# Kernel optimization log

Measured on AMD Instinct MI355X. Metric: run time of the kernel, lower is better.

Reference implementation:

```python
import jax, jax.numpy as jnp
import numpy as np
from jax import lax

B, CI, CO, H, W = 8, 128, 256, 56, 56
P, K = 9, 3  # num_paths, kernel_size


def setup_inputs() -> dict:
    key = jax.random.key(0)
    ks = jax.random.split(key, 7)
    s_conv = 1.0 / np.sqrt(CI * K * K)
    s_o1 = 1.0 / np.sqrt(CI)
    s_o2 = 1.0 / np.sqrt(CO // 2)
    return {
        "x": jax.random.normal(ks[0], (B, CI, H, W), dtype=jnp.float32),
        # num_paths independent 3x3 convs, stacked on leading axis
        "kw": jax.random.uniform(ks[1], (P, CO, CI, K, K), jnp.float32, -s_conv, s_conv),
        "kb": jax.random.uniform(ks[2], (P, CO), jnp.float32, -s_conv, s_conv),
        # observer: 1x1 conv CI -> CO//2, tanh, 1x1 conv CO//2 -> P
        "ow1": jax.random.uniform(ks[3], (CO // 2, CI), jnp.float32, -s_o1, s_o1),
        "ob1": jax.random.uniform(ks[4], (CO // 2,), jnp.float32, -s_o1, s_o1),
        "ow2": jax.random.uniform(ks[5], (P, CO // 2), jnp.float32, -s_o2, s_o2),
        "ob2": jax.random.uniform(ks[6], (P,), jnp.float32, -s_o2, s_o2),
    }


def reference(x, kw, kb, ow1, ob1, ow2, ob2):
    p, co, ci, k, _ = kw.shape
    b, _, h, w = x.shape
    # All num_paths convs as a single grouped-output conv: (P*CO, CI, K, K)
    wflat = kw.reshape(p * co, ci, k, k)
    paths = lax.conv_general_dilated(
        x, wflat, window_strides=(1, 1), padding=((1, 1), (1, 1)),
        dimension_numbers=("NCHW", "OIHW", "NCHW"))
    paths = paths + kb.reshape(p * co)[None, :, None, None]
    paths = paths.reshape(b, p, co, h, w)  # [B,P,CO,H,W]

    # observer: two 1x1 convs (pure channel mixes) with tanh in between
    hmid = jnp.tanh(jnp.einsum("bchw,dc->bdhw", x, ow1) + ob1[None, :, None, None])
    scores = jnp.einsum("bdhw,pd->bphw", hmid, ow2) + ob2[None, :, None, None]

    # eval-mode collapse: argmax over paths, pixel-wise hard selection.
    # (one-hot multiply + sum over paths == gather of the winning path)
    idx = jnp.argmax(scores, axis=1)  # [B,H,W]
    out = jnp.take_along_axis(paths, idx[:, None, None, :, :], axis=1)[:, 0]  # [B,CO,H,W]
    return jax.nn.relu(out)  # norm_type='none' -> identity norm
```

## Files before the change

### kernel.cpp

```cpp
#include <hip/hip_runtime.h>
#include <hip/hip_bf16.h>


typedef unsigned int u32;

#define NPIX    25088
#define XPAD_DW (8*58*58*64)
#define OFF_LIST 4096
#define OFF_XPAD 907264
#define OFF_W2   (907264 + 6889472)

__device__ __forceinline__ unsigned short f2bf(float f) {
  u32 u = __builtin_bit_cast(u32, f);
  u32 r = (u + 0x7FFFu + ((u >> 16) & 1u)) >> 16;
  return (unsigned short)r;
}

#define GLDS16(g, l)                                                        \
  __builtin_amdgcn_global_load_lds(                                         \
      (const __attribute__((address_space(1))) u32*)(g),                    \
      (__attribute__((address_space(3))) u32*)(l), 16, 0, 0)

typedef __attribute__((ext_vector_type(8))) short bf16x8;
typedef __attribute__((ext_vector_type(4))) float f32x4;

__global__ __launch_bounds__(512) void k_front(
    const float* __restrict__ x, const float* __restrict__ kw,
    const float* __restrict__ ow1, const float* __restrict__ ob1,
    const float* __restrict__ ow2, const float* __restrict__ ob2,
    u32* __restrict__ xpad, u32* __restrict__ w2,
    int* __restrict__ cnt, int* __restrict__ list) {
  __shared__ float red[8][64][9];
  __shared__ int lcnt[9], lbase[9];

  int bid = blockIdx.x;
  int tid = threadIdx.x;

  if (bid < 392) {
    int px = tid & 63;
    int dg = tid >> 6;
    int dgu = __builtin_amdgcn_readfirstlane(dg);
    int pix = bid * 64 + px;
    int b = pix / 3136, s = pix - b * 3136;
    const float* xb = x + (size_t)b * 401408 + s;

    if (tid < 9) lcnt[tid] = 0;

    float h[16];
    const float* o1 = ob1 + dgu * 16;
#pragma unroll
    for (int i = 0; i < 16; ++i) h[i] = o1[i];

    const float* w1b = ow1 + dgu * 16 * 128;
    for (int cc = 0; cc < 128; cc += 8) {
      float xc[8];
#pragma unroll
      for (int j = 0; j < 8; ++j) xc[j] = xb[(size_t)(cc + j) * 3136];
#pragma unroll
      for (int i = 0; i < 16; ++i) {
        const float* wr = w1b + i * 128 + cc;
        float a = h[i];
#pragma unroll
        for (int j = 0; j < 8; ++j) a = fmaf(wr[j], xc[j], a);
        h[i] = a;
      }
    }

#pragma unroll
    for (int i = 0; i < 16; ++i) h[i] = tanhf(h[i]);

#pragma unroll
    for (int p = 0; p < 9; ++p) {
      float sc = 0.f;
      const float* wr = ow2 + p * 128 + dgu * 16;
#pragma unroll
      for (int i = 0; i < 16; ++i) sc = fmaf(wr[i], h[i], sc);
      red[dg][px][p] = sc;
    }
    __syncthreads();

    int bi = 0, slot = 0;
    if (dg == 0) {
      float best = 0.f;
#pragma unroll
      for (int p = 0; p < 9; ++p) {
        float v = ob2[p];
#pragma unroll
        for (int g = 0; g < 8; ++g) v += red[g][px][p];
        if (p == 0 || v > best) { best = v; bi = p; }
      }
      slot = atomicAdd(&lcnt[bi], 1);
    }
    __syncthreads();
    if (tid < 9) lbase[tid] = atomicAdd(&cnt[tid], lcnt[tid]);
    __syncthreads();
    if (dg == 0) list[bi * NPIX + lbase[bi] + slot] = pix;

  } else if (bid < 840) {
    int bh = bid - 392;
    int b = bh / 56, hh = bh - b * 56;
    int cp = tid & 63;
    int wq = tid >> 6;
    const float* xb = x + (size_t)(b * 128 + 2 * cp) * 3136 + hh * 56;
    u32* orow = xpad + (size_t)(b * 58 + hh + 1) * 58 * 64;
    for (int w = wq; w < 56; w += 8) {
      float f0 = xb[w];
      float f1 = xb[3136 + w];
      orow[(w + 1) * 64 + cp] = (u32)f2bf(f0) | ((u32)f2bf(f1) << 16);
    }
    if (wq == 0) orow[cp] = 0;
    else if (wq == 1) orow[57 * 64 + cp] = 0;

  } else if (bid < 856) {
    int r = bid - 840;
    int b = r >> 1;
    u32* orow = xpad + ((size_t)(b * 58) + ((r & 1) ? 57 : 0)) * 58 * 64;
    for (int i = tid; i < 58 * 64; i += 512) orow[i] = 0;

  } else {
    for (int t = (bid - 856) * 512 + tid; t < 1327104; t += 256 * 512) {
      int cp = t & 63;
      int r = t >> 6;
      int tap = r % 9;
      int pco = r / 9;
      const float* sp = kw + ((size_t)pco * 128 + 2 * cp) * 9 + tap;
      w2[t] = (u32)f2bf(sp[0]) | ((u32)f2bf(sp[9]) << 16);
    }
  }
}

__global__ __launch_bounds__(256, 3) void k_conv(
    const int* __restrict__ cnt, const int* __restrict__ list,
    const char* __restrict__ xpadB, const char* __restrict__ w2B,
    const float* __restrict__ kb, float* __restrict__ out) {
  __shared__ short Wlds[2][4096];
  __shared__ short Plds[2][4096];
  __shared__ int offsB[128], outSB[128];
  __shared__ float kbl[128];

  int bid = blockIdx.x;
  int half = bid & 1, tb = bid >> 1;
  int p = -1, cntp = 0;
  for (int pp = 0; pp < 9; ++pp) {
    int c = cnt[pp];
    int tt = (c + 127) >> 7;
    if (p < 0) {
      if (tb < tt) { p = pp; cntp = c; }
      else tb -= tt;
    }
  }
  if (p < 0) return;
  int nbase = tb * 128;
  int tid = threadIdx.x;

  if (tid < 128) {
    int g = nbase + tid;
    int pixid = list[p * NPIX + (g < cntp ? g : nbase)];
    int b = pixid / 3136, s = pixid - b * 3136;
    int h = s / 56, w = s - h * 56;
    offsB[tid] = ((b * 58 + h) * 58 + w) * 256;
    outSB[tid] = b * 802816 + s;
    kbl[tid] = kb[p * 256 + half * 128 + tid];
  }
  __syncthreads();

  int seg16 = (tid & 3) * 16;
  int na = tid >> 2;
  int offP0 = offsB[na] + seg16;
  int offP1 = offsB[64 + na] + seg16;
  const char* wrow = w2B + (size_t)(p * 256 + half * 128) * 2304;
  const char* wp0 = wrow + na * 2304 + seg16;
  const char* wp1 = wrow + (size_t)(64 + na) * 2304 + seg16;

  auto stage = [&](int c, int q) {
    int tap = c >> 2, kc = c & 3;
    int wko = tap * 256 + kc * 64;
    int tapoff = ((tap / 3) * 58 + (tap % 3)) * 256 + kc * 64;
    GLDS16(wp0 + wko, &Wlds[q][tid * 8]);
    GLDS16(wp1 + wko, &Wlds[q][2048 + tid * 8]);
    GLDS16(xpadB + (size_t)(offP0 + tapoff), &Plds[q][tid * 8]);
    GLDS16(xpadB + (size_t)(offP1 + tapoff), &Plds[q][2048 + tid * 8]);
  };

  f32x4 acc[4][4];
#pragma unroll
  for (int mt = 0; mt < 4; ++mt)
#pragma unroll
    for (int nt = 0; nt < 4; ++nt) acc[mt][nt] = (f32x4)0.f;

  int lane = tid & 63, wave = tid >> 6;
  int wm = wave >> 1, wn = wave & 1;
  int mrow = wm * 64 + (lane & 15);
  int nrow = wn * 64 + (lane & 15);
  int kg8 = (lane >> 4) * 8;

  stage(0, 0);
  for (int c = 0; c < 36; ++c) {
    __syncthreads();
    if (c + 1 < 36) stage(c + 1, (c + 1) & 1);
    int q = c & 1;
    bf16x8 af[4], bfr[4];
#pragma unroll
    for (int mt = 0; mt < 4; ++mt)
      af[mt] = *(const bf16x8*)&Wlds[q][(mrow + mt * 16) * 32 + kg8];
#pragma unroll
    for (int nt = 0; nt < 4; ++nt)
      bfr[nt] = *(const bf16x8*)&Plds[q][(nrow + nt * 16) * 32 + kg8];
#pragma unroll
    for (int mt = 0; mt < 4; ++mt)
#pragma unroll
      for (int nt = 0; nt < 4; ++nt)
        acc[mt][nt] = __builtin_amdgcn_mfma_f32_16x16x32_bf16(
            af[mt], bfr[nt], acc[mt][nt], 0, 0, 0);
  }

  int col = lane & 15, quad = lane >> 4;
#pragma unroll
  for (int nt = 0; nt < 4; ++nt) {
    int n = wn * 64 + nt * 16 + col;
    bool valid = (nbase + n) < cntp;
    int ob = outSB[n];
#pragma unroll
    for (int mt = 0; mt < 4; ++mt) {
#pragma unroll
      for (int r = 0; r < 4; ++r) {
        int co_l = wm * 64 + mt * 16 + quad * 4 + r;
        float v = acc[mt][nt][r] + kbl[co_l];
        v = v > 0.f ? v : 0.f;
        if (valid) out[ob + (half * 128 + co_l) * 3136] = v;
      }
    }
  }
}

extern "C" void kernel_launch(void* const* d_in, const int* in_sizes, int n_in,
                              void* d_out, int out_size, void* d_ws, size_t ws_size,
                              hipStream_t stream) {
  const float* x   = (const float*)d_in[0];
  const float* kw  = (const float*)d_in[1];
  const float* kb  = (const float*)d_in[2];
  const float* ow1 = (const float*)d_in[3];
  const float* ob1 = (const float*)d_in[4];
  const float* ow2 = (const float*)d_in[5];
  const float* ob2 = (const float*)d_in[6];
  float* out = (float*)d_out;
  char* ws = (char*)d_ws;

  int* cnt  = (int*)(ws);
  int* list = (int*)(ws + OFF_LIST);
  u32* xpad = (u32*)(ws + OFF_XPAD);
  u32* w2   = (u32*)(ws + OFF_W2);

  hipMemsetAsync(cnt, 0, 64, stream);

  k_front<<<1112, 512, 0, stream>>>(x, kw, ow1, ob1, ow2, ob2, xpad, w2,
                                    cnt, list);
  k_conv<<<408, 256, 0, stream>>>(cnt, list, (const char*)xpad, (const char*)w2,
                                  kb, out);
}
```

Baseline: 181.1 us.

## Stage conv results in compact bf16 rows and scatter with a separate coalesced kernel

The conv kernel now writes its output as packed bf16 rows indexed by list position instead of storing fp32 values straight into NCHW. A new k_out kernel uses a pixel-to-row map to read those rows and write the final tensor so that consecutive lanes hit consecutive pixels. The aim is to replace scattered, uncoalesced fp32 stores. The pixel tile also shrinks from 128 to 64, which doubles the block count, and occupancy rises to 4 blocks per CU. LDS reads gain an XOR swizzle to reduce bank conflicts. The cost is an extra launch, an intermediate buffer round trip, and rounding the output to bf16.

```diff
diff --git a/kernel.cpp b/kernel.cpp
--- a/kernel.cpp
+++ b/kernel.cpp
@@ -5,15 +5,22 @@
 typedef unsigned int u32;
 
 #define NPIX    25088
-#define XPAD_DW (8*58*58*64)
 #define OFF_LIST 4096
 #define OFF_XPAD 907264
-#define OFF_W2   (907264 + 6889472)
+#define OFF_W2   7796736
+#define OFF_P2R  13105152
+#define OFF_OUTC 13205504
 
 __device__ __forceinline__ unsigned short f2bf(float f) {
   u32 u = __builtin_bit_cast(u32, f);
   u32 r = (u + 0x7FFFu + ((u >> 16) & 1u)) >> 16;
   return (unsigned short)r;
+}
+__device__ __forceinline__ float bflo(u32 w) {
+  return __builtin_bit_cast(float, w << 16);
+}
+__device__ __forceinline__ float bfhi(u32 w) {
+  return __builtin_bit_cast(float, w & 0xFFFF0000u);
 }
 
 #define GLDS16(g, l)                                                        \
@@ -129,48 +136,50 @@
   }
 }
 
-__global__ __launch_bounds__(256, 3) void k_conv(
+__global__ __launch_bounds__(256, 4) void k_conv(
     const int* __restrict__ cnt, const int* __restrict__ list,
     const char* __restrict__ xpadB, const char* __restrict__ w2B,
-    const float* __restrict__ kb, float* __restrict__ out) {
+    const float* __restrict__ kb, unsigned short* __restrict__ outcH,
+    int* __restrict__ pix2row) {
   __shared__ short Wlds[2][4096];
-  __shared__ short Plds[2][4096];
-  __shared__ int offsB[128], outSB[128];
+  __shared__ short Plds[2][2048];
+  __shared__ int offsB[64];
   __shared__ float kbl[128];
 
   int bid = blockIdx.x;
   int half = bid & 1, tb = bid >> 1;
-  int p = -1, cntp = 0;
+  int p = -1, cntp = 0, baseP = 0, accb = 0;
   for (int pp = 0; pp < 9; ++pp) {
     int c = cnt[pp];
-    int tt = (c + 127) >> 7;
+    int tt = (c + 63) >> 6;
     if (p < 0) {
-      if (tb < tt) { p = pp; cntp = c; }
+      if (tb < tt) { p = pp; cntp = c; baseP = accb; }
       else tb -= tt;
     }
+    accb += c;
   }
   if (p < 0) return;
-  int nbase = tb * 128;
+  int nbase = tb * 64;
   int tid = threadIdx.x;
 
-  if (tid < 128) {
+  if (tid < 64) {
     int g = nbase + tid;
-    int pixid = list[p * NPIX + (g < cntp ? g : nbase)];
+    bool v = g < cntp;
+    int pixid = list[p * NPIX + (v ? g : nbase)];
     int b = pixid / 3136, s = pixid - b * 3136;
     int h = s / 56, w = s - h * 56;
     offsB[tid] = ((b * 58 + h) * 58 + w) * 256;
-    outSB[tid] = b * 802816 + s;
-    kbl[tid] = kb[p * 256 + half * 128 + tid];
-  }
+    if (v && half == 0) pix2row[pixid] = baseP + g;
+  }
+  if (tid < 128) kbl[tid] = kb[p * 256 + half * 128 + tid];
   __syncthreads();
 
-  int seg16 = (tid & 3) * 16;
+  int segsw = ((tid & 3) ^ ((tid >> 3) & 3)) * 16;
   int na = tid >> 2;
-  int offP0 = offsB[na] + seg16;
-  int offP1 = offsB[64 + na] + seg16;
+  int offP = offsB[na] + segsw;
   const char* wrow = w2B + (size_t)(p * 256 + half * 128) * 2304;
-  const char* wp0 = wrow + na * 2304 + seg16;
-  const char* wp1 = wrow + (size_t)(64 + na) * 2304 + seg16;
+  const char* wp0 = wrow + (size_t)na * 2304 + segsw;
+  const char* wp1 = wrow + (size_t)(64 + na) * 2304 + segsw;
 
   auto stage = [&](int c, int q) {
     int tap = c >> 2, kc = c & 3;
@@ -178,58 +187,86 @@
     int tapoff = ((tap / 3) * 58 + (tap % 3)) * 256 + kc * 64;
     GLDS16(wp0 + wko, &Wlds[q][tid * 8]);
     GLDS16(wp1 + wko, &Wlds[q][2048 + tid * 8]);
-    GLDS16(xpadB + (size_t)(offP0 + tapoff), &Plds[q][tid * 8]);
-    GLDS16(xpadB + (size_t)(offP1 + tapoff), &Plds[q][2048 + tid * 8]);
+    GLDS16(xpadB + (size_t)(offP + tapoff), &Plds[q][tid * 8]);
   };
 
-  f32x4 acc[4][4];
+  f32x4 acc[4][2];
 #pragma unroll
   for (int mt = 0; mt < 4; ++mt)
 #pragma unroll
-    for (int nt = 0; nt < 4; ++nt) acc[mt][nt] = (f32x4)0.f;
+    for (int nt = 0; nt < 2; ++nt) acc[mt][nt] = (f32x4)0.f;
 
   int lane = tid & 63, wave = tid >> 6;
   int wm = wave >> 1, wn = wave & 1;
-  int mrow = wm * 64 + (lane & 15);
-  int nrow = wn * 64 + (lane & 15);
-  int kg8 = (lane >> 4) * 8;
+  int l15 = lane & 15, quad = lane >> 4;
+  int slot = (quad ^ ((l15 >> 1) & 3)) * 8;
+  int mrow = wm * 64 + l15;
+  int nrow = wn * 32 + l15;
 
   stage(0, 0);
   for (int c = 0; c < 36; ++c) {
     __syncthreads();
     if (c + 1 < 36) stage(c + 1, (c + 1) & 1);
     int q = c & 1;
-    bf16x8 af[4], bfr[4];
+    bf16x8 af[4], bfr[2];
 #pragma unroll
     for (int mt = 0; mt < 4; ++mt)
-      af[mt] = *(const bf16x8*)&Wlds[q][(mrow + mt * 16) * 32 + kg8];
-#pragma unroll
-    for (int nt = 0; nt < 4; ++nt)
-      bfr[nt] = *(const bf16x8*)&Plds[q][(nrow + nt * 16) * 32 + kg8];
+      af[mt] = *(const bf16x8*)&Wlds[q][(mrow + mt * 16) * 32 + slot];
+#pragma unroll
+    for (int nt = 0; nt < 2; ++nt)
+      bfr[nt] = *(const bf16x8*)&Plds[q][(nrow + nt * 16) * 32 + slot];
 #pragma unroll
     for (int mt = 0; mt < 4; ++mt)
 #pragma unroll
-      for (int nt = 0; nt < 4; ++nt)
+      for (int nt = 0; nt < 2; ++nt)
         acc[mt][nt] = __builtin_amdgcn_mfma_f32_16x16x32_bf16(
             af[mt], bfr[nt], acc[mt][nt], 0, 0, 0);
   }
 
-  int col = lane & 15, quad = lane >> 4;
-#pragma unroll
-  for (int nt = 0; nt < 4; ++nt) {
-    int n = wn * 64 + nt * 16 + col;
-    bool valid = (nbase + n) < cntp;
-    int ob = outSB[n];
+#pragma unroll
+  for (int nt = 0; nt < 2; ++nt) {
+    int n = wn * 32 + nt * 16 + l15;
+    if ((nbase + n) >= cntp) continue;
+    size_t rowb = (size_t)(baseP + nbase + n) * 256 + half * 128;
 #pragma unroll
     for (int mt = 0; mt < 4; ++mt) {
-#pragma unroll
-      for (int r = 0; r < 4; ++r) {
-        int co_l = wm * 64 + mt * 16 + quad * 4 + r;
-        float v = acc[mt][nt][r] + kbl[co_l];
-        v = v > 0.f ? v : 0.f;
-        if (valid) out[ob + (half * 128 + co_l) * 3136] = v;
-      }
-    }
+      int co0 = wm * 64 + mt * 16 + quad * 4;
+      float v0 = acc[mt][nt][0] + kbl[co0 + 0];
+      float v1 = acc[mt][nt][1] + kbl[co0 + 1];
+      float v2 = acc[mt][nt][2] + kbl[co0 + 2];
+      float v3 = acc[mt][nt][3] + kbl[co0 + 3];
+      v0 = v0 > 0.f ? v0 : 0.f;  v1 = v1 > 0.f ? v1 : 0.f;
+      v2 = v2 > 0.f ? v2 : 0.f;  v3 = v3 > 0.f ? v3 : 0.f;
+      u32 lo = (u32)f2bf(v0) | ((u32)f2bf(v1) << 16);
+      u32 hi = (u32)f2bf(v2) | ((u32)f2bf(v3) << 16);
+      *(u32*)&outcH[rowb + co0]     = lo;
+      *(u32*)&outcH[rowb + co0 + 2] = hi;
+    }
+  }
+}
+
+__global__ __launch_bounds__(256) void k_out(
+    const int* __restrict__ pix2row, const u32* __restrict__ outcU,
+    float* __restrict__ out) {
+  int tid = threadIdx.x;
+  int pl = tid & 63, coq = tid >> 6;
+  int pix = blockIdx.x * 64 + pl;
+  int b = pix / 3136, s = pix - b * 3136;
+  int row = pix2row[pix];
+  const u32* src = outcU + (size_t)row * 128 + coq * 32;
+  float* dst = out + (size_t)b * 802816 + s;
+#pragma unroll
+  for (int j = 0; j < 8; ++j) {
+    uint4 w = *(const uint4*)(src + j * 4);
+    int co = coq * 64 + j * 8;
+    dst[(size_t)(co + 0) * 3136] = bflo(w.x);
+    dst[(size_t)(co + 1) * 3136] = bfhi(w.x);
+    dst[(size_t)(co + 2) * 3136] = bflo(w.y);
+    dst[(size_t)(co + 3) * 3136] = bfhi(w.y);
+    dst[(size_t)(co + 4) * 3136] = bflo(w.z);
+    dst[(size_t)(co + 5) * 3136] = bfhi(w.z);
+    dst[(size_t)(co + 6) * 3136] = bflo(w.w);
+    dst[(size_t)(co + 7) * 3136] = bfhi(w.w);
   }
 }
 
@@ -250,11 +287,14 @@
   int* list = (int*)(ws + OFF_LIST);
   u32* xpad = (u32*)(ws + OFF_XPAD);
   u32* w2   = (u32*)(ws + OFF_W2);
+  int* p2r  = (int*)(ws + OFF_P2R);
+  unsigned short* outc = (unsigned short*)(ws + OFF_OUTC);
 
   hipMemsetAsync(cnt, 0, 64, stream);
 
   k_front<<<1112, 512, 0, stream>>>(x, kw, ow1, ob1, ow2, ob2, xpad, w2,
                                     cnt, list);
-  k_conv<<<408, 256, 0, stream>>>(cnt, list, (const char*)xpad, (const char*)w2,
-                                  kb, out);
-}
+  k_conv<<<802, 256, 0, stream>>>(cnt, list, (const char*)xpad, (const char*)w2,
+                                  kb, outc, p2r);
+  k_out<<<392, 256, 0, stream>>>(p2r, (const u32*)outc, out);
+}
```

New measurement: 165.4 us. -8.6%, faster.
